# Kernel tuning notes

Hardware: AMD Instinct MI355X
Metric: run time of the kernel (lower is better)

## Reference

```python
import jax, jax.numpy as jnp
import numpy as np

N = 50000      # nodes
E = 1_600_000  # edges (avg degree 32)
G = 2000       # graphs in batch
H = 2          # attention heads
C = 64         # out_channels
IN = 64        # in_channels
NEG_SLOPE = 0.2


def setup_inputs() -> dict:
    key = jax.random.key(0)
    ks = jax.random.split(key, 6)
    x = jax.random.normal(ks[0], (N, IN), dtype=jnp.float32)
    edge_index = jax.random.randint(ks[1], (2, E), 0, N, dtype=jnp.int32)
    batch = jnp.sort(jax.random.randint(ks[2], (N,), 0, G, dtype=jnp.int32))
    # GATConv params: lin weight [H*C, IN] (glorot-ish), att vectors, bias [C]
    W = jax.random.normal(ks[3], (H * C, IN), dtype=jnp.float32) * (1.0 / np.sqrt(IN))
    att_src = jax.random.normal(ks[4], (1, H, C), dtype=jnp.float32) * 0.1
    att_dst = jax.random.normal(ks[5], (1, H, C), dtype=jnp.float32) * 0.1
    bias = jnp.zeros((C,), dtype=jnp.float32)
    return {"x": x, "edge_index": edge_index, "batch": batch,
            "W": W, "att_src": att_src, "att_dst": att_dst, "bias": bias}


def reference(x, edge_index, batch, W, att_src, att_dst, bias):
    # --- GATConv (PyG semantics: add_self_loops=True, concat=False -> head mean + bias) ---
    loops = jnp.arange(N, dtype=edge_index.dtype)
    src = jnp.concatenate([edge_index[0], loops])  # [E+N]
    dst = jnp.concatenate([edge_index[1], loops])  # [E+N]

    xp = (x @ W.T).reshape(N, H, C)                 # projected node feats [N,H,C]
    a_src = jnp.sum(xp * att_src, axis=-1)          # [N,H]
    a_dst = jnp.sum(xp * att_dst, axis=-1)          # [N,H]

    e = jax.nn.leaky_relu(a_src[src] + a_dst[dst], NEG_SLOPE)  # [E+N,H]
    # segment softmax over incoming edges of each destination node
    m = jax.ops.segment_max(e, dst, num_segments=N)            # [N,H]
    e = jnp.exp(e - m[dst])
    s = jax.ops.segment_sum(e, dst, num_segments=N)            # [N,H]
    alpha = e / s[dst]                                         # [E+N,H]

    msg = xp[src] * alpha[:, :, None]                          # [E+N,H,C]
    out = jax.ops.segment_sum(msg, dst, num_segments=N)        # [N,H,C]
    h_nodes = out.mean(axis=1) + bias                          # [N,C]

    # --- global_mean_pool ---
    sums = jax.ops.segment_sum(h_nodes, batch, num_segments=G)                     # [G,C]
    cnt = jax.ops.segment_sum(jnp.ones((N, 1), h_nodes.dtype), batch, num_segments=G)
    h_graphs = sums / jnp.maximum(cnt, 1.0)                                        # [G,C]
    return (h_nodes, h_graphs)
```

## Files before the change

### kernel.cpp

```cpp
#include <hip/hip_runtime.h>
#include <hip/hip_bf16.h>

#define H 2
#define C 64
#define IN_CH 64
#define HC (H*C)
#define NEG_SLOPE 0.2f
#define NBUCK_MAX 512
#define SBLK 512
#define CHUNK_MAX 3136
#define CAP 6144

__global__ __launch_bounds__(128) void proj_kernel(
    const float* __restrict__ x, const float* __restrict__ W,
    const float* __restrict__ att_src, const float* __restrict__ att_dst,
    const int* __restrict__ batch, __hip_bfloat16* __restrict__ xp,
    float* __restrict__ asrc, float* __restrict__ adst, int* __restrict__ cnt,
    int* __restrict__ gbeg, int N, int nbuck, int G) {
    int t = threadIdx.x;
    if (blockIdx.x == 0)
        for (int i = t; i < nbuck; i += 128) cnt[i] = 0;
    {
        int i = blockIdx.x * 128 + t;
        if (i < N) {
            int bi = batch[i];
            if (i == 0) {
                for (int g = 0; g <= bi; g++) gbeg[g] = 0;
            } else {
                int bp = batch[i - 1];
                for (int g = bp + 1; g <= bi; g++) gbeg[g] = i;
            }
            if (i == N - 1)
                for (int g = bi + 1; g <= G; g++) gbeg[g] = N;
        }
    }
    float w[64];
    const float4* wr = reinterpret_cast<const float4*>(W + (size_t)t * IN_CH);
#pragma unroll
    for (int q = 0; q < 16; q++) {
        float4 v = wr[q];
        w[4 * q] = v.x; w[4 * q + 1] = v.y; w[4 * q + 2] = v.z; w[4 * q + 3] = v.w;
    }
    float a_s = att_src[t], a_d = att_dst[t];
    int lane = t & 63, head = t >> 6;
    for (int n = blockIdx.x; n < N; n += gridDim.x) {
        const float* xr = x + (size_t)n * IN_CH;
        float acc = 0.f;
#pragma unroll
        for (int k = 0; k < 64; k++) acc = fmaf(w[k], xr[k], acc);
        xp[(size_t)n * HC + t] = __float2bfloat16(acc);
        float as = acc * a_s, ad = acc * a_d;
#pragma unroll
        for (int d = 32; d > 0; d >>= 1) {
            as += __shfl_xor(as, d, 64);
            ad += __shfl_xor(ad, d, 64);
        }
        if (lane == 0) {
            asrc[(size_t)n * H + head] = as;
            adst[(size_t)n * H + head] = ad;
        }
    }
}

__global__ __launch_bounds__(256) void scatter_kernel(
    const int* __restrict__ edge, int* __restrict__ cnt,
    int* __restrict__ staged, int N, int E) {
    const int tid = threadIdx.x, bid = blockIdx.x;
    const int nbuck = (N + 127) >> 7;
    const int chunkE = (E + SBLK - 1) / SBLK;
    const int* srcE = edge;
    const int* dstE = edge + E;
    __shared__ int2 eds[CHUNK_MAX];
    __shared__ int lh[NBUCK_MAX], bse[NBUCK_MAX], lcur[NBUCK_MAX];
    for (int i = tid; i < nbuck; i += 256) { lh[i] = 0; lcur[i] = 0; }
    __syncthreads();
    int beg = bid * chunkE, end = min(beg + chunkE, E);
    int m = end - beg;
    for (int i = tid; i < m; i += 256) {
        int s = srcE[beg + i], d = dstE[beg + i];
        eds[i] = make_int2(s, d);
        atomicAdd(&lh[d >> 7], 1);
    }
    __syncthreads();
    for (int i = tid; i < nbuck; i += 256)
        bse[i] = atomicAdd(&cnt[i], lh[i]);
    __syncthreads();
    for (int i = tid; i < m; i += 256) {
        int2 e = eds[i];
        int b = e.y >> 7;
        int l = atomicAdd(&lcur[b], 1);
        staged[(size_t)b * CAP + bse[b] + l] = e.x | ((e.y & 127) << 20);
    }
}

__global__ __launch_bounds__(512) void bucket_csr_kernel(
    const int* __restrict__ staged, const int* __restrict__ cnt,
    int* __restrict__ off, int* __restrict__ csr, int N, int nbuck) {
    int b = blockIdx.x, t = threadIdx.x;
    __shared__ int bse[512], rs[512], lh[128], sh[128], cur[128];
    {
        int v = (t < nbuck) ? cnt[t] : 0;
        bse[t] = v; rs[t] = v;
        __syncthreads();
        for (int d = 1; d < 512; d <<= 1) {
            int u = (t >= d) ? bse[t - d] : 0;
            __syncthreads();
            bse[t] += u;
            __syncthreads();
        }
        bse[t] -= rs[t];
        __syncthreads();
    }
    int base = bse[b], size = rs[b];
    const int* st = staged + (size_t)b * CAP;
    if (t < 128) lh[t] = 0;
    __syncthreads();
    for (int i = t; i < size; i += 512)
        atomicAdd(&lh[st[i] >> 20], 1);
    __syncthreads();
    int v = (t < 128) ? lh[t] : 0;
    if (t < 128) sh[t] = v;
    __syncthreads();
    for (int d = 1; d < 128; d <<= 1) {
        int u = (t >= d && t < 128) ? sh[t - d] : 0;
        __syncthreads();
        if (t < 128) sh[t] += u;
        __syncthreads();
    }
    if (t < 128) {
        int ex = sh[t] - v;
        int nd = b * 128 + t;
        if (nd < N) off[nd] = base + ex;
        if (nd == N - 1) off[N] = base + size;
        cur[t] = base + ex;
    }
    __syncthreads();
    for (int i = t; i < size; i += 512) {
        int e = st[i];
        int pos = atomicAdd(&cur[e >> 20], 1);
        csr[pos] = e & 0xFFFFF;
    }
}

template<int NB16>
__device__ __forceinline__ void gather_fma(const uint* __restrict__ xpw,
                                           const int* __restrict__ sidx,
                                           const float2* __restrict__ swt,
                                           int lane, float& accx, float& accy) {
    uint bu[NB16 * 16];
#pragma unroll
    for (int j = 0; j < NB16 * 16; j++) {
        int s2 = sidx[j];
        bu[j] = xpw[(size_t)s2 * 64 + lane];
    }
#pragma unroll
    for (int j = 0; j < NB16 * 16; j++) {
        float2 wv = swt[j];
        float wgt = (lane < 32) ? wv.x : wv.y;
        accx = fmaf(wgt, __uint_as_float(bu[j] << 16), accx);
        accy = fmaf(wgt, __uint_as_float(bu[j] & 0xffff0000u), accy);
    }
}

__global__ __launch_bounds__(256, 4) void aggregate_kernel(
    const __hip_bfloat16* __restrict__ xp, const float2* __restrict__ asrc,
    const float2* __restrict__ adst, const int* __restrict__ off,
    const int* __restrict__ csr, const float* __restrict__ bias,
    float* __restrict__ out, int N) {
    __shared__ int sidx[4][64];
    __shared__ float2 swt[4][64];
    int wid = threadIdx.x >> 6;
    int n = blockIdx.x * 4 + wid;
    if (n >= N) return;
    int lane = threadIdx.x & 63;
    int* si = sidx[wid];
    float2* sw = swt[wid];
    int o0 = off[n];
    int degE = off[n + 1] - o0;
    float2 ad = adst[n];
    float2 asn = asrc[n];
    float es0 = asn.x + ad.x; es0 = (es0 > 0.f) ? es0 : NEG_SLOPE * es0;
    float es1 = asn.y + ad.y; es1 = (es1 > 0.f) ? es1 : NEG_SLOPE * es1;
    float ws0 = __expf(es0), ws1 = __expf(es1);
    float s0 = (lane == 0) ? ws0 : 0.f;
    float s1 = (lane == 0) ? ws1 : 0.f;

    const uint* xpw = reinterpret_cast<const uint*>(xp);
    float accx, accy;
    {
        float wgt = (lane < 32) ? ws0 : ws1;
        uint u = xpw[(size_t)n * 64 + lane];
        accx = wgt * __uint_as_float(u << 16);
        accy = wgt * __uint_as_float(u & 0xffff0000u);
    }

    for (int base = 0; base < degE; base += 64) {
        int i = base + lane;
        int idx = 0;
        float w0 = 0.f, w1 = 0.f;
        if (i < degE) {
            idx = csr[o0 + i];
            float2 as = asrc[idx];
            float t0 = as.x + ad.x; t0 = (t0 > 0.f) ? t0 : NEG_SLOPE * t0;
            float t1 = as.y + ad.y; t1 = (t1 > 0.f) ? t1 : NEG_SLOPE * t1;
            w0 = __expf(t0);
            w1 = __expf(t1);
        }
        s0 += w0;
        s1 += w1;
        si[lane] = idx;
        sw[lane] = make_float2(w0, w1);
        int cnt2 = min(degE - base, 64);
        int nb16 = (cnt2 + 15) >> 4;
        switch (nb16) {
            case 1: gather_fma<1>(xpw, si, sw, lane, accx, accy); break;
            case 2: gather_fma<2>(xpw, si, sw, lane, accx, accy); break;
            case 3: gather_fma<3>(xpw, si, sw, lane, accx, accy); break;
            default: gather_fma<4>(xpw, si, sw, lane, accx, accy); break;
        }
    }
#pragma unroll
    for (int d = 32; d > 0; d >>= 1) {
        s0 += __shfl_xor(s0, d, 64);
        s1 += __shfl_xor(s1, d, 64);
    }
    float inv = (lane < 32) ? (1.f / s0) : (1.f / s1);
    accx *= inv;
    accy *= inv;
    float ox = 0.5f * (accx + __shfl_xor(accx, 32, 64));
    float oy = 0.5f * (accy + __shfl_xor(accy, 32, 64));
    if (lane < 32) {
        float vx = ox + bias[2 * lane];
        float vy = oy + bias[2 * lane + 1];
        *reinterpret_cast<float2*>(out + (size_t)n * C + 2 * lane) = make_float2(vx, vy);
    }
}

__global__ __launch_bounds__(256) void pool_kernel(const float* __restrict__ hn,
                                                   const int* __restrict__ gbeg,
                                                   float* __restrict__ outG, int G) {
    int g = blockIdx.x;
    int c = threadIdx.x & 63, r = threadIdx.x >> 6;
    int beg = gbeg[g], end = gbeg[g + 1];
    float s = 0.f;
    for (int n = beg + r; n < end; n += 4) s += hn[(size_t)n * C + c];
    __shared__ float red[256];
    red[threadIdx.x] = s;
    __syncthreads();
    if (r == 0) {
        float tot = red[c] + red[64 + c] + red[128 + c] + red[192 + c];
        outG[(size_t)g * C + c] = tot / fmaxf((float)(end - beg), 1.f);
    }
}

extern "C" void kernel_launch(void* const* d_in, const int* in_sizes, int n_in,
                              void* d_out, int out_size, void* d_ws, size_t ws_size,
                              hipStream_t stream) {
    const float* x       = (const float*)d_in[0];
    const int*   edge    = (const int*)d_in[1];
    const int*   batch   = (const int*)d_in[2];
    const float* W       = (const float*)d_in[3];
    const float* att_src = (const float*)d_in[4];
    const float* att_dst = (const float*)d_in[5];
    const float* bias    = (const float*)d_in[6];

    int N = in_sizes[0] / IN_CH;
    int E = in_sizes[1] / 2;
    int G = out_size / C - N;
    int nbuck = (N + 127) >> 7;

    char* p = (char*)d_ws;
    auto alloc = [&](size_t bytes) {
        char* r = p;
        p += (bytes + 255) & ~(size_t)255;
        return r;
    };
    __hip_bfloat16* xp = (__hip_bfloat16*)alloc((size_t)N * HC * 2);
    float* asrc    = (float*)alloc((size_t)N * H * 4);
    float* adst    = (float*)alloc((size_t)N * H * 4);
    int*   cnt     = (int*)alloc((size_t)nbuck * 4);
    int*   off     = (int*)alloc((size_t)(N + 1) * 4);
    int*   staged  = (int*)alloc((size_t)nbuck * CAP * 4);
    int*   csr     = (int*)alloc((size_t)E * 4);
    int*   gbeg    = (int*)alloc((size_t)(G + 1) * 4);

    proj_kernel<<<2048, 128, 0, stream>>>(x, W, att_src, att_dst, batch, xp, asrc, adst,
                                          cnt, gbeg, N, nbuck, G);
    scatter_kernel<<<SBLK, 256, 0, stream>>>(edge, cnt, staged, N, E);
    bucket_csr_kernel<<<nbuck, 512, 0, stream>>>(staged, cnt, off, csr, N, nbuck);
    aggregate_kernel<<<(N + 3) / 4, 256, 0, stream>>>(xp, (const float2*)asrc,
                                                      (const float2*)adst, off, csr, bias,
                                                      (float*)d_out, N);
    pool_kernel<<<G, 256, 0, stream>>>((const float*)d_out, gbeg,
                                       (float*)d_out + (size_t)N * C, G);
}
```

Before: 206.7 us.

## Split aggregate wave per head, pad bucket counters, double scatter blocks

The aggregate kernel now gives each half-wave one attention head. The 32 lanes of a half compute edge weights for 32 edges at a time, so the redundant two-head exp work per lane goes away. Gathers use precomputed byte offsets (idx<<8), and the batch size becomes 16 or 32 edges instead of 16–64. Bucket counters are padded to a 16-int stride to cut atomic contention and false sharing, and the scatter kernel uses twice as many blocks with smaller chunks. The trade-off is more loop iterations for high-degree nodes and fewer loads in flight per batch.

```diff
diff --git a/kernel.cpp b/kernel.cpp
--- a/kernel.cpp
+++ b/kernel.cpp
@@ -7,9 +7,10 @@
 #define HC (H*C)
 #define NEG_SLOPE 0.2f
 #define NBUCK_MAX 512
-#define SBLK 512
-#define CHUNK_MAX 3136
+#define SBLK 1024
+#define CHUNK_MAX 1600
 #define CAP 6144
+#define CNT_STRIDE 16
 
 __global__ __launch_bounds__(128) void proj_kernel(
     const float* __restrict__ x, const float* __restrict__ W,
@@ -19,7 +20,7 @@
     int* __restrict__ gbeg, int N, int nbuck, int G) {
     int t = threadIdx.x;
     if (blockIdx.x == 0)
-        for (int i = t; i < nbuck; i += 128) cnt[i] = 0;
+        for (int i = t; i < nbuck; i += 128) cnt[i * CNT_STRIDE] = 0;
     {
         int i = blockIdx.x * 128 + t;
         if (i < N) {
@@ -83,7 +84,7 @@
     }
     __syncthreads();
     for (int i = tid; i < nbuck; i += 256)
-        bse[i] = atomicAdd(&cnt[i], lh[i]);
+        bse[i] = atomicAdd(&cnt[i * CNT_STRIDE], lh[i]);
     __syncthreads();
     for (int i = tid; i < m; i += 256) {
         int2 e = eds[i];
@@ -99,7 +100,7 @@
     int b = blockIdx.x, t = threadIdx.x;
     __shared__ int bse[512], rs[512], lh[128], sh[128], cur[128];
     {
-        int v = (t < nbuck) ? cnt[t] : 0;
+        int v = (t < nbuck) ? cnt[t * CNT_STRIDE] : 0;
         bse[t] = v; rs[t] = v;
         __syncthreads();
         for (int d = 1; d < 512; d <<= 1) {
@@ -142,97 +143,86 @@
     }
 }
 
-template<int NB16>
-__device__ __forceinline__ void gather_fma(const uint* __restrict__ xpw,
-                                           const int* __restrict__ sidx,
-                                           const float2* __restrict__ swt,
-                                           int lane, float& accx, float& accy) {
-    uint bu[NB16 * 16];
-#pragma unroll
-    for (int j = 0; j < NB16 * 16; j++) {
-        int s2 = sidx[j];
-        bu[j] = xpw[(size_t)s2 * 64 + lane];
-    }
-#pragma unroll
-    for (int j = 0; j < NB16 * 16; j++) {
-        float2 wv = swt[j];
-        float wgt = (lane < 32) ? wv.x : wv.y;
-        accx = fmaf(wgt, __uint_as_float(bu[j] << 16), accx);
-        accy = fmaf(wgt, __uint_as_float(bu[j] & 0xffff0000u), accy);
+template<int NB>
+__device__ __forceinline__ void gfma(const uint* __restrict__ xpw,
+                                     const int* __restrict__ si,
+                                     const float* __restrict__ swl,
+                                     uint laneoff, float& accx, float& accy) {
+    const char* xb = reinterpret_cast<const char*>(xpw);
+    uint bu[NB];
+#pragma unroll
+    for (int j = 0; j < NB; j++) {
+        uint boff = (uint)si[j] + laneoff;
+        bu[j] = *reinterpret_cast<const uint*>(xb + boff);
+    }
+#pragma unroll
+    for (int j = 0; j < NB; j++) {
+        float w = swl[2 * j];
+        accx = fmaf(w, __uint_as_float(bu[j] << 16), accx);
+        accy = fmaf(w, __uint_as_float(bu[j] & 0xffff0000u), accy);
     }
 }
 
 __global__ __launch_bounds__(256, 4) void aggregate_kernel(
-    const __hip_bfloat16* __restrict__ xp, const float2* __restrict__ asrc,
-    const float2* __restrict__ adst, const int* __restrict__ off,
+    const __hip_bfloat16* __restrict__ xp, const float* __restrict__ asrc,
+    const float* __restrict__ adst, const int* __restrict__ off,
     const int* __restrict__ csr, const float* __restrict__ bias,
     float* __restrict__ out, int N) {
-    __shared__ int sidx[4][64];
-    __shared__ float2 swt[4][64];
+    __shared__ int sidx[4][32];
+    __shared__ float swf[4][64];
     int wid = threadIdx.x >> 6;
     int n = blockIdx.x * 4 + wid;
     if (n >= N) return;
     int lane = threadIdx.x & 63;
+    int cl = lane & 31;
+    int hsel = lane >> 5;
     int* si = sidx[wid];
-    float2* sw = swt[wid];
+    float* swl = swf[wid] + hsel;
     int o0 = off[n];
-    int degE = off[n + 1] - o0;
-    float2 ad = adst[n];
-    float2 asn = asrc[n];
-    float es0 = asn.x + ad.x; es0 = (es0 > 0.f) ? es0 : NEG_SLOPE * es0;
-    float es1 = asn.y + ad.y; es1 = (es1 > 0.f) ? es1 : NEG_SLOPE * es1;
-    float ws0 = __expf(es0), ws1 = __expf(es1);
-    float s0 = (lane == 0) ? ws0 : 0.f;
-    float s1 = (lane == 0) ? ws1 : 0.f;
+    int deg = off[n + 1] - o0;
+    float adh = adst[2 * n + hsel];
+    float es = asrc[2 * n + hsel] + adh;
+    es = (es > 0.f) ? es : NEG_SLOPE * es;
+    float wself = __expf(es);
+    float ssum = (cl == 0) ? wself : 0.f;
 
     const uint* xpw = reinterpret_cast<const uint*>(xp);
+    uint laneoff = (uint)lane * 4u;
     float accx, accy;
     {
-        float wgt = (lane < 32) ? ws0 : ws1;
         uint u = xpw[(size_t)n * 64 + lane];
-        accx = wgt * __uint_as_float(u << 16);
-        accy = wgt * __uint_as_float(u & 0xffff0000u);
-    }
-
-    for (int base = 0; base < degE; base += 64) {
-        int i = base + lane;
+        accx = wself * __uint_as_float(u << 16);
+        accy = wself * __uint_as_float(u & 0xffff0000u);
+    }
+
+    for (int base = 0; base < deg; base += 32) {
+        int i = base + cl;
         int idx = 0;
-        float w0 = 0.f, w1 = 0.f;
-        if (i < degE) {
+        float w = 0.f;
+        if (i < deg) {
             idx = csr[o0 + i];
-            float2 as = asrc[idx];
-            float t0 = as.x + ad.x; t0 = (t0 > 0.f) ? t0 : NEG_SLOPE * t0;
-            float t1 = as.y + ad.y; t1 = (t1 > 0.f) ? t1 : NEG_SLOPE * t1;
-            w0 = __expf(t0);
-            w1 = __expf(t1);
-        }
-        s0 += w0;
-        s1 += w1;
-        si[lane] = idx;
-        sw[lane] = make_float2(w0, w1);
-        int cnt2 = min(degE - base, 64);
-        int nb16 = (cnt2 + 15) >> 4;
-        switch (nb16) {
-            case 1: gather_fma<1>(xpw, si, sw, lane, accx, accy); break;
-            case 2: gather_fma<2>(xpw, si, sw, lane, accx, accy); break;
-            case 3: gather_fma<3>(xpw, si, sw, lane, accx, accy); break;
-            default: gather_fma<4>(xpw, si, sw, lane, accx, accy); break;
-        }
-    }
-#pragma unroll
-    for (int d = 32; d > 0; d >>= 1) {
-        s0 += __shfl_xor(s0, d, 64);
-        s1 += __shfl_xor(s1, d, 64);
-    }
-    float inv = (lane < 32) ? (1.f / s0) : (1.f / s1);
+            float t = asrc[2 * idx + hsel] + adh;
+            t = (t > 0.f) ? t : NEG_SLOPE * t;
+            w = __expf(t);
+        }
+        ssum += w;
+        si[cl] = idx << 8;
+        swl[2 * cl] = w;
+        int nb = min(deg - base, 32);
+        if (nb > 16) gfma<32>(xpw, si, swl, laneoff, accx, accy);
+        else         gfma<16>(xpw, si, swl, laneoff, accx, accy);
+    }
+#pragma unroll
+    for (int d = 16; d > 0; d >>= 1) ssum += __shfl_xor(ssum, d, 64);
+    float inv = 1.f / ssum;
     accx *= inv;
     accy *= inv;
     float ox = 0.5f * (accx + __shfl_xor(accx, 32, 64));
     float oy = 0.5f * (accy + __shfl_xor(accy, 32, 64));
     if (lane < 32) {
-        float vx = ox + bias[2 * lane];
-        float vy = oy + bias[2 * lane + 1];
-        *reinterpret_cast<float2*>(out + (size_t)n * C + 2 * lane) = make_float2(vx, vy);
+        float vx = ox + bias[2 * cl];
+        float vy = oy + bias[2 * cl + 1];
+        *reinterpret_cast<float2*>(out + (size_t)n * C + 2 * cl) = make_float2(vx, vy);
     }
 }
 
@@ -278,7 +268,7 @@
     __hip_bfloat16* xp = (__hip_bfloat16*)alloc((size_t)N * HC * 2);
     float* asrc    = (float*)alloc((size_t)N * H * 4);
     float* adst    = (float*)alloc((size_t)N * H * 4);
-    int*   cnt     = (int*)alloc((size_t)nbuck * 4);
+    int*   cnt     = (int*)alloc((size_t)nbuck * CNT_STRIDE * 4);
     int*   off     = (int*)alloc((size_t)(N + 1) * 4);
     int*   staged  = (int*)alloc((size_t)nbuck * CAP * 4);
     int*   csr     = (int*)alloc((size_t)E * 4);
@@ -288,8 +278,7 @@
                                           cnt, gbeg, N, nbuck, G);
     scatter_kernel<<<SBLK, 256, 0, stream>>>(edge, cnt, staged, N, E);
     bucket_csr_kernel<<<nbuck, 512, 0, stream>>>(staged, cnt, off, csr, N, nbuck);
-    aggregate_kernel<<<(N + 3) / 4, 256, 0, stream>>>(xp, (const float2*)asrc,
-                                                      (const float2*)adst, off, csr, bias,
+    aggregate_kernel<<<(N + 3) / 4, 256, 0, stream>>>(xp, asrc, adst, off, csr, bias,
                                                       (float*)d_out, N);
     pool_kernel<<<G, 256, 0, stream>>>((const float*)d_out, gbeg,
                                        (float*)d_out + (size_t)N * C, G);
```

Measured after the change: 223.4 us. +8.1%, slower.
